# Optimization experiments

Hardware: AMD Instinct MI355X
Metric: run time of the kernel (lower is better)

Reference implementation:

```python
import jax, jax.numpy as jnp
import numpy as np

B, C, INTER, H, W = 4, 256, 128, 64, 64
EPS = 1e-5

def conv1x1(x, w, b):
    # x: [B,Cin,H,W], w: [Cout,Cin], b: [Cout]
    return jnp.einsum('bchw,oc->bohw', x, w) + b[None, :, None, None]

def setup_inputs() -> dict:
    key = jax.random.key(0)
    ks = jax.random.split(key, 12)
    sc_in = 1.0 / np.sqrt(C)
    sc_int = 1.0 / np.sqrt(INTER)
    return {
        'x': jax.random.normal(ks[0], (B, C, H, W), dtype=jnp.float32),
        'g_w': jax.random.normal(ks[1], (INTER, C), dtype=jnp.float32) * sc_in,
        'g_b': jax.random.normal(ks[2], (INTER,), dtype=jnp.float32) * 0.01,
        'theta_w': jax.random.normal(ks[3], (INTER, C), dtype=jnp.float32) * sc_in,
        'theta_b': jax.random.normal(ks[4], (INTER,), dtype=jnp.float32) * 0.01,
        'phi_w': jax.random.normal(ks[5], (INTER, C), dtype=jnp.float32) * sc_in,
        'phi_b': jax.random.normal(ks[6], (INTER,), dtype=jnp.float32) * 0.01,
        'w_w': jax.random.normal(ks[7], (C, INTER), dtype=jnp.float32) * sc_int,
        'w_b': jax.random.normal(ks[8], (C,), dtype=jnp.float32) * 0.01,
        'gamma': jax.random.normal(ks[9], (C,), dtype=jnp.float32) * 0.1 + 1.0,
        'beta': jax.random.normal(ks[10], (C,), dtype=jnp.float32) * 0.1,
    }

def reference(x, g_w, g_b, theta_w, theta_b, phi_w, phi_b, w_w, w_b, gamma, beta):
    b, c, h, w = x.shape
    n = h * w
    g_x = conv1x1(x, g_w, g_b).reshape(b, INTER, n).transpose(0, 2, 1)      # [b,n,d]
    theta_x = conv1x1(x, theta_w, theta_b).reshape(b, INTER, n).transpose(0, 2, 1)  # [b,n,d]
    phi_x = conv1x1(x, phi_w, phi_b).reshape(b, INTER, n)                   # [b,d,n]
    f = jnp.einsum('bnd,bdm->bnm', theta_x, phi_x)                          # [b,n,n]
    f_div_c = jax.nn.softmax(f, axis=-1)
    y = jnp.einsum('bnm,bmd->bnd', f_div_c, g_x)                            # [b,n,d]
    y = y.transpose(0, 2, 1).reshape(b, INTER, h, w)                        # [b,d,h,w]
    w_y = conv1x1(y, w_w, w_b)                                              # [b,c,h,w]
    # BatchNorm2d (training mode: batch statistics, biased variance)
    mean = jnp.mean(w_y, axis=(0, 2, 3), keepdims=True)
    var = jnp.var(w_y, axis=(0, 2, 3), keepdims=True)
    bn = (w_y - mean) * jax.lax.rsqrt(var + EPS)
    bn = bn * gamma[None, :, None, None] + beta[None, :, None, None]
    return bn + x
```

## Files before the change

kernel.cpp:

```cpp
#include <hip/hip_runtime.h>

#define B_ 4
#define C_ 256
#define D_ 128
#define N_ 4096
#define BN_ 16384

typedef unsigned short u16t;
typedef _Float16 f16t;
typedef f16t f16x8 __attribute__((ext_vector_type(8)));
typedef f16t f16x4 __attribute__((ext_vector_type(4)));
typedef float f32x4 __attribute__((ext_vector_type(4)));

static __device__ __forceinline__ u16t f2h(float f) {
  f16t h = (f16t)f; u16t u; __builtin_memcpy(&u, &h, 2); return u;
}
static __device__ __forceinline__ float h2f(u16t u) {
  f16t h; __builtin_memcpy(&h, &u, 2); return (float)h;
}

static __device__ __forceinline__ void gld_lds16(const u16t* g, u16t* l) {
  __builtin_amdgcn_global_load_lds(
      (const __attribute__((address_space(1))) void*)g,
      (__attribute__((address_space(3))) void*)l, 16, 0, 0);
}

__global__ __launch_bounds__(256) void transpose_prep(
    const float* __restrict__ x, u16t* __restrict__ xT,
    const float* __restrict__ th_w, const float* __restrict__ ph_w,
    const float* __restrict__ th_b, const float* __restrict__ ph_b,
    const float* __restrict__ g_w, const float* __restrict__ w_w,
    u16t* __restrict__ Wc, u16t* __restrict__ gwc, u16t* __restrict__ wwc,
    float* __restrict__ bc) {
  __shared__ u16t t[32][33];
  const int b = blockIdx.z, c0 = blockIdx.y * 32, n0 = blockIdx.x * 32;
  const int tid = threadIdx.x;
  {
    const int cl = tid >> 3, n4 = (tid & 7) * 4;
    const float4 v = *(const float4*)(x + ((size_t)b * C_ + c0 + cl) * N_ + n0 + n4);
    t[n4 + 0][cl] = f2h(v.x);
    t[n4 + 1][cl] = f2h(v.y);
    t[n4 + 2][cl] = f2h(v.z);
    t[n4 + 3][cl] = f2h(v.w);
  }
  __syncthreads();
  {
    const int nl = tid >> 3, c4 = (tid & 7) * 4;
    unsigned int lo = (unsigned int)t[nl][c4 + 0] | ((unsigned int)t[nl][c4 + 1] << 16);
    unsigned int hi = (unsigned int)t[nl][c4 + 2] | ((unsigned int)t[nl][c4 + 3] << 16);
    uint2 o; o.x = lo; o.y = hi;
    *(uint2*)(xT + ((size_t)b * N_ + n0 + nl) * C_ + c0 + c4) = o;
  }
  if (blockIdx.y == 0 && blockIdx.z == 0) {
    for (int idx = blockIdx.x * 256 + tid; idx < 131328; idx += 32768) {
      if (idx < 65536) {
        const int j = idx >> 8, c = idx & 255;
        const float v = (j < 128) ? th_w[j * 256 + c] : ph_w[(j - 128) * 256 + c];
        Wc[idx] = f2h(v);
      } else if (idx < 98304) {
        const int i = idx - 65536;
        gwc[i] = f2h(g_w[i]);
      } else if (idx < 131072) {
        const int i = idx - 98304;
        wwc[i] = f2h(w_w[i]);
      } else {
        const int j = idx - 131072;
        bc[j] = (j < 128) ? th_b[j] : ph_b[j - 128];
      }
    }
  }
}

__global__ __launch_bounds__(256)
void gemm_qkv(const u16t* __restrict__ xT, const u16t* __restrict__ Wc,
              const u16t* __restrict__ gwc, const float* __restrict__ bc,
              const float* __restrict__ g_b, u16t* __restrict__ QKo,
              u16t* __restrict__ Vo) {
  __shared__ __attribute__((aligned(16))) u16t lA[128 * 40];
  __shared__ __attribute__((aligned(16))) u16t lB[128 * 40];
  const int z = blockIdx.z, bx = blockIdx.x;
  const u16t* xTb = xT + (size_t)z * N_ * C_;
  const u16t* A; const u16t* B; u16t* Cb; int ldc, m0, j0, colb;
  const float* bias;
  if (bx < 64) {
    A = xTb; B = Wc; Cb = QKo + (size_t)z * N_ * 256; ldc = 256;
    m0 = (bx >> 1) * 128; j0 = (bx & 1) * 128; bias = bc; colb = 1;
  } else {
    A = gwc; B = xTb; Cb = Vo + (size_t)z * D_ * N_; ldc = N_;
    m0 = 0; j0 = (bx - 64) * 128; bias = g_b; colb = 0;
  }
  const int tid = threadIdx.x, lane = tid & 63, wave = tid >> 6;
  const int quad = lane >> 4, l16 = lane & 15;
  const int wm = wave & 1, wj = wave >> 1;

  const f32x4 zero = {0.f, 0.f, 0.f, 0.f};
  f32x4 acc[4][4];
#pragma unroll
  for (int mi = 0; mi < 4; ++mi)
#pragma unroll
    for (int ji = 0; ji < 4; ++ji) acc[mi][ji] = zero;

  for (int k0 = 0; k0 < 256; k0 += 32) {
#pragma unroll
    for (int rr = 0; rr < 2; ++rr) {
      const int idx = rr * 256 + tid;
      const int row = idx >> 2, sg = idx & 3;
      *(uint4*)&lA[row * 40 + sg * 8] = *(const uint4*)(A + (size_t)(m0 + row) * 256 + k0 + sg * 8);
      *(uint4*)&lB[row * 40 + sg * 8] = *(const uint4*)(B + (size_t)(j0 + row) * 256 + k0 + sg * 8);
    }
    __syncthreads();
    f16x8 af[4], bfr[4];
#pragma unroll
    for (int i = 0; i < 4; ++i)
      af[i] = *(const f16x8*)&lA[(wm * 64 + i * 16 + l16) * 40 + quad * 8];
#pragma unroll
    for (int i = 0; i < 4; ++i)
      bfr[i] = *(const f16x8*)&lB[(wj * 64 + i * 16 + l16) * 40 + quad * 8];
#pragma unroll
    for (int mi = 0; mi < 4; ++mi)
#pragma unroll
      for (int ji = 0; ji < 4; ++ji)
        acc[mi][ji] = __builtin_amdgcn_mfma_f32_16x16x32_f16(af[mi], bfr[ji], acc[mi][ji], 0, 0, 0);
    __syncthreads();
  }

  float cb[4];
  if (colb) {
#pragma unroll
    for (int ji = 0; ji < 4; ++ji) cb[ji] = bias[j0 + wj * 64 + ji * 16 + l16];
  }
#pragma unroll
  for (int mi = 0; mi < 4; ++mi) {
#pragma unroll
    for (int r = 0; r < 4; ++r) {
      const int row = m0 + wm * 64 + mi * 16 + quad * 4 + r;
      const float rb = colb ? 0.f : bias[row];
#pragma unroll
      for (int ji = 0; ji < 4; ++ji) {
        const int col = j0 + wj * 64 + ji * 16 + l16;
        const float v = acc[mi][ji][r] + (colb ? cb[ji] : rb);
        Cb[(size_t)row * ldc + col] = f2h(v);
      }
    }
  }
}

__global__ __launch_bounds__(256, 2)
void attn(const u16t* __restrict__ QK, const u16t* __restrict__ V,
          u16t* __restrict__ On0, u16t* __restrict__ On1, float* __restrict__ ml) {
  const int b = blockIdx.y;
  const int split = blockIdx.z;
  const int n0 = blockIdx.x * 128;
  const int kv0 = split * (N_ / 4);
  const int tid = threadIdx.x, lane = tid & 63, wave = tid >> 6;
  const int quad = lane >> 4, l16 = lane & 15;
  const int x7 = l16 & 7;
  __shared__ __attribute__((aligned(16))) u16t Ks[2][64 * 128];
  __shared__ __attribute__((aligned(16))) u16t Vs[2][128 * 64];
  const u16t* QKb = QK + (size_t)b * N_ * 256;
  const u16t* Vb  = V  + (size_t)b * D_ * N_;

  const int krow_l = lane >> 4, kchunk_l = lane & 15;
  const int vrow_l = lane >> 3, vchunk_l = lane & 7;

  f16x8 qf[2][4];
#pragma unroll
  for (int qi = 0; qi < 2; ++qi) {
    const u16t* qrow = QKb + (size_t)(n0 + wave * 32 + qi * 16 + l16) * 256;
#pragma unroll
    for (int kc = 0; kc < 4; ++kc)
      qf[qi][kc] = *(const f16x8*)(qrow + kc * 32 + quad * 8);
  }

  const f32x4 zero = {0.f, 0.f, 0.f, 0.f};
  f32x4 o[2][8];
#pragma unroll
  for (int qi = 0; qi < 2; ++qi)
#pragma unroll
    for (int db = 0; db < 8; ++db) o[qi][db] = zero;
  float m[2] = {-1e30f, -1e30f}, l[2] = {0.f, 0.f};

#pragma unroll
  for (int i = 0; i < 4; ++i) {
    const int krow = (wave * 4 + i) * 4 + krow_l;
    const int kcl = kchunk_l ^ (krow & 7);
    gld_lds16(QKb + (size_t)(kv0 + krow) * 256 + 128 + kcl * 8,
              &Ks[0][(wave * 4 + i) * 512]);
  }
#pragma unroll
  for (int i = 0; i < 4; ++i) {
    const int vrow = (wave * 4 + i) * 8 + vrow_l;
    const int vcl = vchunk_l ^ (vrow & 7);
    gld_lds16(Vb + (size_t)vrow * N_ + kv0 + vcl * 8,
              &Vs[0][(wave * 4 + i) * 512]);
  }
  __syncthreads();

  int cur = 0;
  for (int it = 0; it < 16; ++it) {
    if (it < 15) {
      const int kvn = kv0 + (it + 1) * 64;
#pragma unroll
      for (int i = 0; i < 4; ++i) {
        const int krow = (wave * 4 + i) * 4 + krow_l;
        const int kcl = kchunk_l ^ (krow & 7);
        gld_lds16(QKb + (size_t)(kvn + krow) * 256 + 128 + kcl * 8,
                  &Ks[cur ^ 1][(wave * 4 + i) * 512]);
      }
#pragma unroll
      for (int i = 0; i < 4; ++i) {
        const int vrow = (wave * 4 + i) * 8 + vrow_l;
        const int vcl = vchunk_l ^ (vrow & 7);
        gld_lds16(Vb + (size_t)vrow * N_ + kvn + vcl * 8,
                  &Vs[cur ^ 1][(wave * 4 + i) * 512]);
      }
    }

    const u16t* KsC = &Ks[cur][0];
    const u16t* VsC = &Vs[cur][0];

    f32x4 s[2][4];
#pragma unroll
    for (int qi = 0; qi < 2; ++qi)
#pragma unroll
      for (int ci = 0; ci < 4; ++ci) s[qi][ci] = zero;
#pragma unroll
    for (int kc = 0; kc < 4; ++kc) {
#pragma unroll
      for (int ci = 0; ci < 4; ++ci) {
        f16x8 kf = *(const f16x8*)&KsC[(ci * 16 + l16) * 128 + (((kc * 4 + quad) ^ x7) << 3)];
        s[0][ci] = __builtin_amdgcn_mfma_f32_16x16x32_f16(kf, qf[0][kc], s[0][ci], 0, 0, 0);
        s[1][ci] = __builtin_amdgcn_mfma_f32_16x16x32_f16(kf, qf[1][kc], s[1][ci], 0, 0, 0);
      }
    }

    f16x4 pb[2][4];
#pragma unroll
    for (int qi = 0; qi < 2; ++qi) {
      float m0_ = fmaxf(fmaxf(s[qi][0][0], s[qi][0][1]), fmaxf(s[qi][0][2], s[qi][0][3]));
      float m1_ = fmaxf(fmaxf(s[qi][1][0], s[qi][1][1]), fmaxf(s[qi][1][2], s[qi][1][3]));
      float m2_ = fmaxf(fmaxf(s[qi][2][0], s[qi][2][1]), fmaxf(s[qi][2][2], s[qi][2][3]));
      float m3_ = fmaxf(fmaxf(s[qi][3][0], s[qi][3][1]), fmaxf(s[qi][3][2], s[qi][3][3]));
      float mx = fmaxf(fmaxf(m0_, m1_), fmaxf(m2_, m3_));
      mx = fmaxf(mx, __shfl_xor(mx, 16));
      mx = fmaxf(mx, __shfl_xor(mx, 32));
      const bool defer = __all(mx <= m[qi] + 8.f);
      float mnew = m[qi];
      if (!defer) {
        mnew = fmaxf(m[qi], mx);
        const float alq = __expf(m[qi] - mnew);
        l[qi] *= alq;
#pragma unroll
        for (int db = 0; db < 8; ++db) {
#pragma unroll
          for (int r = 0; r < 4; ++r) o[qi][db][r] *= alq;
        }
        m[qi] = mnew;
      }
      float psum = 0.f;
#pragma unroll
      for (int ci = 0; ci < 4; ++ci) {
#pragma unroll
        for (int r = 0; r < 4; ++r) {
          const float p = __expf(s[qi][ci][r] - mnew);
          psum += p;
          pb[qi][ci][r] = (f16t)p;
        }
      }
      psum += __shfl_xor(psum, 16);
      psum += __shfl_xor(psum, 32);
      l[qi] += psum;
    }

#pragma unroll
    for (int ci = 0; ci < 4; ++ci) {
#pragma unroll
      for (int db = 0; db < 8; ++db) {
        f16x4 av = *(const f16x4*)&VsC[(db * 16 + l16) * 64 +
                                       (((ci * 2 + (quad >> 1)) ^ x7) << 3) + (quad & 1) * 4];
        o[0][db] = __builtin_amdgcn_mfma_f32_16x16x16f16(av, pb[0][ci], o[0][db], 0, 0, 0);
        o[1][db] = __builtin_amdgcn_mfma_f32_16x16x16f16(av, pb[1][ci], o[1][db], 0, 0, 0);
      }
    }
    __syncthreads();
    cur ^= 1;
  }

  u16t* Onb = (split < 2) ? On0 : On1;
  const int sp = split & 1;
#pragma unroll
  for (int qi = 0; qi < 2; ++qi) {
    const int q = n0 + wave * 32 + qi * 16 + l16;
    const float inv = 1.0f / l[qi];
    u16t* yrow = Onb + (((size_t)sp * B_ + b) * N_ + q) * D_;
#pragma unroll
    for (int db = 0; db < 8; ++db) {
      f16x4 pk;
#pragma unroll
      for (int r = 0; r < 4; ++r) pk[r] = (f16t)(o[qi][db][r] * inv);
      *(f16x4*)(yrow + db * 16 + quad * 4) = pk;
    }
    if (quad == 0) {
      float* mlp = ml + ((size_t)split * BN_ + (size_t)b * N_ + q) * 2;
      mlp[0] = m[qi]; mlp[1] = l[qi];
    }
  }
}

__global__ __launch_bounds__(256)
void gemm_wy(const u16t* __restrict__ wwc, const u16t* __restrict__ O0,
             const u16t* __restrict__ O2, const float* __restrict__ ml,
             u16t* __restrict__ wy, const float* __restrict__ w_b) {
  __shared__ __attribute__((aligned(16))) u16t lA[4][128 * 40];
  __shared__ __attribute__((aligned(16))) u16t lB[4][64 * 40];
  __shared__ float wrow[64][4];
  const int z = blockIdx.z;
  const int m0 = blockIdx.y * 128, j0 = blockIdx.x * 64;
  const int tid = threadIdx.x, lane = tid & 63, wave = tid >> 6;
  const int quad = lane >> 4, l16 = lane & 15;
  const int wm = wave & 1, wj = wave >> 1;
  const size_t halfO = (size_t)BN_ * D_;

  uint4 b0[4], b1[4], b2[4], b3[4];
#pragma unroll
  for (int cs = 0; cs < 4; ++cs) {
    const int cid = cs * 256 + tid;
    const int row = cid >> 4, sg = cid & 15;
    const size_t base = ((size_t)z * N_ + j0 + row) * D_ + sg * 8;
    b0[cs] = *(const uint4*)(O0 + base);
    b1[cs] = *(const uint4*)(O0 + halfO + base);
    b2[cs] = *(const uint4*)(O2 + base);
    b3[cs] = *(const uint4*)(O2 + halfO + base);
  }
  uint4 aw[8];
#pragma unroll
  for (int as = 0; as < 8; ++as) {
    const int cid = as * 256 + tid;
    const int row = cid >> 4, sg = cid & 15;
    aw[as] = *(const uint4*)(wwc + (size_t)(m0 + row) * 128 + sg * 8);
  }
  float mlv[8];
  if (tid < 64) {
    const int q = j0 + tid;
#pragma unroll
    for (int s = 0; s < 4; ++s) {
      mlv[2 * s]     = ml[((size_t)s * BN_ + (size_t)z * N_ + q) * 2];
      mlv[2 * s + 1] = ml[((size_t)s * BN_ + (size_t)z * N_ + q) * 2 + 1];
    }
  }
  if (tid < 64) {
    float mstar = -1e30f;
#pragma unroll
    for (int s = 0; s < 4; ++s) mstar = fmaxf(mstar, mlv[2 * s]);
    float w[4], wsum = 0.f;
#pragma unroll
    for (int s = 0; s < 4; ++s) { w[s] = __expf(mlv[2 * s] - mstar) * mlv[2 * s + 1]; wsum += w[s]; }
    const float inv = 1.0f / wsum;
#pragma unroll
    for (int s = 0; s < 4; ++s) wrow[tid][s] = w[s] * inv;
  }
#pragma unroll
  for (int as = 0; as < 8; ++as) {
    const int cid = as * 256 + tid;
    const int row = cid >> 4, sg = cid & 15;
    *(uint4*)&lA[sg >> 2][row * 40 + (sg & 3) * 8] = aw[as];
  }
  __syncthreads();
#pragma unroll
  for (int cs = 0; cs < 4; ++cs) {
    const int cid = cs * 256 + tid;
    const int row = cid >> 4, sg = cid & 15;
    const float w0 = wrow[row][0], w1 = wrow[row][1];
    const float w2 = wrow[row][2], w3 = wrow[row][3];
    const unsigned* p0 = &b0[cs].x; const unsigned* p1 = &b1[cs].x;
    const unsigned* p2 = &b2[cs].x; const unsigned* p3 = &b3[cs].x;
    uint4 y; unsigned* py = &y.x;
#pragma unroll
    for (int i = 0; i < 4; ++i) {
      const float lo = w0 * h2f((u16t)(p0[i] & 0xffff)) + w1 * h2f((u16t)(p1[i] & 0xffff)) +
                       w2 * h2f((u16t)(p2[i] & 0xffff)) + w3 * h2f((u16t)(p3[i] & 0xffff));
      const float hi = w0 * h2f((u16t)(p0[i] >> 16)) + w1 * h2f((u16t)(p1[i] >> 16)) +
                       w2 * h2f((u16t)(p2[i] >> 16)) + w3 * h2f((u16t)(p3[i] >> 16));
      py[i] = (unsigned)f2h(lo) | ((unsigned)f2h(hi) << 16);
    }
    *(uint4*)&lB[sg >> 2][row * 40 + (sg & 3) * 8] = y;
  }
  __syncthreads();

  const f32x4 zero = {0.f, 0.f, 0.f, 0.f};
  f32x4 acc[4][2];
#pragma unroll
  for (int mi = 0; mi < 4; ++mi)
#pragma unroll
    for (int ji = 0; ji < 2; ++ji) acc[mi][ji] = zero;
#pragma unroll
  for (int kc = 0; kc < 4; ++kc) {
    f16x8 af[4], bfr[2];
#pragma unroll
    for (int i = 0; i < 4; ++i)
      af[i] = *(const f16x8*)&lA[kc][(wm * 64 + i * 16 + l16) * 40 + quad * 8];
#pragma unroll
    for (int i = 0; i < 2; ++i)
      bfr[i] = *(const f16x8*)&lB[kc][(wj * 32 + i * 16 + l16) * 40 + quad * 8];
#pragma unroll
    for (int mi = 0; mi < 4; ++mi)
#pragma unroll
      for (int ji = 0; ji < 2; ++ji)
        acc[mi][ji] = __builtin_amdgcn_mfma_f32_16x16x32_f16(af[mi], bfr[ji], acc[mi][ji], 0, 0, 0);
  }

#pragma unroll
  for (int mi = 0; mi < 4; ++mi) {
#pragma unroll
    for (int r = 0; r < 4; ++r) {
      const int row = m0 + wm * 64 + mi * 16 + quad * 4 + r;
      const float rb = w_b[row];
#pragma unroll
      for (int ji = 0; ji < 2; ++ji) {
        const int col = j0 + wj * 32 + ji * 16 + l16;
        const float v = acc[mi][ji][r] + rb;
        wy[(size_t)z * C_ * N_ + (size_t)row * N_ + col] = f2h(v);
      }
    }
  }
}

__global__ __launch_bounds__(256) void bn_stats_fin(const u16t* __restrict__ wy,
                                                    const float* __restrict__ x,
                                                    const float* __restrict__ gamma,
                                                    const float* __restrict__ beta,
                                                    float* __restrict__ out) {
  const int c = blockIdx.x;
  const int tid = threadIdx.x, lane = tid & 63, wave = tid >> 6;
  __shared__ float red[8];
  __shared__ float mv[2];
  float s1 = 0.f, s2 = 0.f;
#pragma unroll
  for (int it = 0; it < 8; ++it) {
    const int e = (it * 256 + tid) * 8;
    const int z = e >> 12, n = e & 4095;
    const uint4 v = *(const uint4*)(wy + (size_t)z * C_ * N_ + (size_t)c * N_ + n);
    const unsigned* p = &v.x;
#pragma unroll
    for (int i = 0; i < 4; ++i) {
      const float lo = h2f((u16t)(p[i] & 0xffff));
      const float hi = h2f((u16t)(p[i] >> 16));
      s1 += lo + hi;
      s2 += lo * lo + hi * hi;
    }
  }
  s1 += __shfl_xor(s1, 1);  s2 += __shfl_xor(s2, 1);
  s1 += __shfl_xor(s1, 2);  s2 += __shfl_xor(s2, 2);
  s1 += __shfl_xor(s1, 4);  s2 += __shfl_xor(s2, 4);
  s1 += __shfl_xor(s1, 8);  s2 += __shfl_xor(s2, 8);
  s1 += __shfl_xor(s1, 16); s2 += __shfl_xor(s2, 16);
  s1 += __shfl_xor(s1, 32); s2 += __shfl_xor(s2, 32);
  if (lane == 0) { red[wave] = s1; red[4 + wave] = s2; }
  __syncthreads();
  if (tid == 0) {
    const float inv_n = 1.0f / 16384.0f;
    const float tot1 = red[0] + red[1] + red[2] + red[3];
    const float tot2 = red[4] + red[5] + red[6] + red[7];
    const float mean = tot1 * inv_n;
    const float var = tot2 * inv_n - mean * mean;
    mv[0] = mean;
    mv[1] = rsqrtf(var + 1e-5f);
  }
  __syncthreads();
  const float mean = mv[0], rs = mv[1];
  const float g = gamma[c], bt = beta[c];
#pragma unroll
  for (int it = 0; it < 16; ++it) {
    const int e4 = it * 256 + tid;
    const int z = e4 >> 10, n4 = (e4 & 1023) * 4;
    const size_t off = ((size_t)z * C_ + c) * N_ + n4;
    const uint2 wv = *(const uint2*)(wy + off);
    const float4 xv = *(const float4*)(x + off);
    float4 ov;
    ov.x = (h2f((u16t)(wv.x & 0xffff)) - mean) * rs * g + bt + xv.x;
    ov.y = (h2f((u16t)(wv.x >> 16))    - mean) * rs * g + bt + xv.y;
    ov.z = (h2f((u16t)(wv.y & 0xffff)) - mean) * rs * g + bt + xv.z;
    ov.w = (h2f((u16t)(wv.y >> 16))    - mean) * rs * g + bt + xv.w;
    *(float4*)(out + off) = ov;
  }
}

extern "C" void kernel_launch(void* const* d_in, const int* in_sizes, int n_in,
                              void* d_out, int out_size, void* d_ws, size_t ws_size,
                              hipStream_t stream) {
  const float* x     = (const float*)d_in[0];
  const float* g_w   = (const float*)d_in[1];
  const float* g_b   = (const float*)d_in[2];
  const float* th_w  = (const float*)d_in[3];
  const float* th_b  = (const float*)d_in[4];
  const float* ph_w  = (const float*)d_in[5];
  const float* ph_b  = (const float*)d_in[6];
  const float* w_w   = (const float*)d_in[7];
  const float* w_b   = (const float*)d_in[8];
  const float* gamma = (const float*)d_in[9];
  const float* beta  = (const float*)d_in[10];
  float* out = (float*)d_out;
  char* ws = (char*)d_ws;

  u16t* O0  = (u16t*)(ws);
  u16t* QK  = (u16t*)(ws + 8388608);
  u16t* wy  = (u16t*)(ws + 8388608);
  u16t* V   = (u16t*)(ws + 16777216);
  u16t* Wc  = (u16t*)(ws + 20971520);
  u16t* gwc = (u16t*)(ws + 21102592);
  u16t* wwc = (u16t*)(ws + 21168128);
  float* bc = (float*)(ws + 21233664);
  float* ml = (float*)(ws + 21236736);
  u16t* O2 = (u16t*)d_out;

  transpose_prep<<<dim3(128, 8, B_), dim3(256), 0, stream>>>(
      x, (u16t*)ws, th_w, ph_w, th_b, ph_b, g_w, w_w, Wc, gwc, wwc, bc);

  gemm_qkv<<<dim3(96, 1, B_), dim3(256), 0, stream>>>(
      (u16t*)ws, Wc, gwc, bc, g_b, QK, V);

  attn<<<dim3(32, B_, 4), dim3(256), 0, stream>>>(QK, V, O0, O2, ml);

  gemm_wy<<<dim3(64, 2, B_), dim3(256), 0, stream>>>(wwc, O0, O2, ml, wy, w_b);

  bn_stats_fin<<<dim3(256), dim3(256), 0, stream>>>(wy, x, gamma, beta, out);
}
```

Baseline: 167.7 us.

## Fuse all five stages into one cooperative persistent kernel with grid syncs

Result: slower. 432.7 us (+158.0%).

```diff
diff --git a/kernel.cpp b/kernel.cpp
--- a/kernel.cpp
+++ b/kernel.cpp
@@ -1,4 +1,7 @@
 #include <hip/hip_runtime.h>
+#include <hip/hip_cooperative_groups.h>
+
+namespace cg = cooperative_groups;
 
 #define B_ 4
 #define C_ 256
@@ -23,6 +26,463 @@
   __builtin_amdgcn_global_load_lds(
       (const __attribute__((address_space(1))) void*)g,
       (__attribute__((address_space(3))) void*)l, 16, 0, 0);
+}
+
+__global__ __launch_bounds__(256, 2) void mega(
+    const float* __restrict__ x,
+    const float* __restrict__ th_w, const float* __restrict__ ph_w,
+    const float* __restrict__ th_b, const float* __restrict__ ph_b,
+    const float* __restrict__ g_w, const float* __restrict__ g_b,
+    const float* __restrict__ w_w, const float* __restrict__ w_b,
+    const float* __restrict__ gamma, const float* __restrict__ beta,
+    float* out,
+    u16t* xT,
+    u16t* QK,
+    u16t* __restrict__ V,
+    u16t* __restrict__ Wc, u16t* __restrict__ gwc, u16t* __restrict__ wwc,
+    float* __restrict__ bc, float* __restrict__ ml,
+    u16t* O2) {
+  __shared__ __attribute__((aligned(16))) char smem[65536];
+  cg::grid_group gg = cg::this_grid();
+  const int fblk = blockIdx.x;
+  const int tid = threadIdx.x, lane = tid & 63, wave = tid >> 6;
+  const int quad = lane >> 4, l16 = lane & 15;
+  const int wm = wave & 1, wj = wave >> 1;
+  const f32x4 zero = {0.f, 0.f, 0.f, 0.f};
+
+  if (fblk < 128) {
+    for (int idx = fblk * 256 + tid; idx < 131328; idx += 32768) {
+      if (idx < 65536) {
+        const int j = idx >> 8, c = idx & 255;
+        const float v = (j < 128) ? th_w[j * 256 + c] : ph_w[(j - 128) * 256 + c];
+        Wc[idx] = f2h(v);
+      } else if (idx < 98304) {
+        gwc[idx - 65536] = f2h(g_w[idx - 65536]);
+      } else if (idx < 131072) {
+        wwc[idx - 98304] = f2h(w_w[idx - 98304]);
+      } else {
+        const int j = idx - 131072;
+        bc[j] = (j < 128) ? th_b[j] : ph_b[j - 128];
+      }
+    }
+  }
+  {
+    u16t (*t)[33] = (u16t (*)[33])smem;
+    for (int i = 0; i < 8; ++i) {
+      const int tt = i * 512 + fblk;
+      const int bx = tt & 127, by = (tt >> 7) & 7, bz = tt >> 10;
+      const int c0 = by * 32, n0 = bx * 32;
+      {
+        const int cl = tid >> 3, n4 = (tid & 7) * 4;
+        const float4 v = *(const float4*)(x + ((size_t)bz * C_ + c0 + cl) * N_ + n0 + n4);
+        t[n4 + 0][cl] = f2h(v.x);
+        t[n4 + 1][cl] = f2h(v.y);
+        t[n4 + 2][cl] = f2h(v.z);
+        t[n4 + 3][cl] = f2h(v.w);
+      }
+      __syncthreads();
+      {
+        const int nl = tid >> 3, c4 = (tid & 7) * 4;
+        unsigned lo = (unsigned)t[nl][c4 + 0] | ((unsigned)t[nl][c4 + 1] << 16);
+        unsigned hi = (unsigned)t[nl][c4 + 2] | ((unsigned)t[nl][c4 + 3] << 16);
+        uint2 o; o.x = lo; o.y = hi;
+        *(uint2*)(xT + ((size_t)bz * N_ + n0 + nl) * C_ + c0 + c4) = o;
+      }
+      __syncthreads();
+    }
+  }
+  gg.sync();
+
+  if (fblk < 384) {
+    u16t* lA = (u16t*)smem;
+    u16t* lB = (u16t*)(smem + 10240);
+    const int z = fblk / 96, bx = fblk % 96;
+    const u16t* xTb = xT + (size_t)z * N_ * C_;
+    const u16t* A; const u16t* B; u16t* Cb; int ldc, m0, j0, colb;
+    const float* bias;
+    if (bx < 64) {
+      A = xTb; B = Wc; Cb = QK + (size_t)z * N_ * 256; ldc = 256;
+      m0 = (bx >> 1) * 128; j0 = (bx & 1) * 128; bias = bc; colb = 1;
+    } else {
+      A = gwc; B = xTb; Cb = V + (size_t)z * D_ * N_; ldc = N_;
+      m0 = 0; j0 = (bx - 64) * 128; bias = g_b; colb = 0;
+    }
+    f32x4 acc[4][4];
+#pragma unroll
+    for (int mi = 0; mi < 4; ++mi)
+#pragma unroll
+      for (int ji = 0; ji < 4; ++ji) acc[mi][ji] = zero;
+
+    for (int k0 = 0; k0 < 256; k0 += 32) {
+#pragma unroll
+      for (int rr = 0; rr < 2; ++rr) {
+        const int idx = rr * 256 + tid;
+        const int row = idx >> 2, sg = idx & 3;
+        *(uint4*)&lA[row * 40 + sg * 8] = *(const uint4*)(A + (size_t)(m0 + row) * 256 + k0 + sg * 8);
+        *(uint4*)&lB[row * 40 + sg * 8] = *(const uint4*)(B + (size_t)(j0 + row) * 256 + k0 + sg * 8);
+      }
+      __syncthreads();
+      f16x8 af[4], bfr[4];
+#pragma unroll
+      for (int i = 0; i < 4; ++i)
+        af[i] = *(const f16x8*)&lA[(wm * 64 + i * 16 + l16) * 40 + quad * 8];
+#pragma unroll
+      for (int i = 0; i < 4; ++i)
+        bfr[i] = *(const f16x8*)&lB[(wj * 64 + i * 16 + l16) * 40 + quad * 8];
+#pragma unroll
+      for (int mi = 0; mi < 4; ++mi)
+#pragma unroll
+        for (int ji = 0; ji < 4; ++ji)
+          acc[mi][ji] = __builtin_amdgcn_mfma_f32_16x16x32_f16(af[mi], bfr[ji], acc[mi][ji], 0, 0, 0);
+      __syncthreads();
+    }
+
+    float cb[4];
+    if (colb) {
+#pragma unroll
+      for (int ji = 0; ji < 4; ++ji) cb[ji] = bias[j0 + wj * 64 + ji * 16 + l16];
+    }
+#pragma unroll
+    for (int mi = 0; mi < 4; ++mi) {
+#pragma unroll
+      for (int r = 0; r < 4; ++r) {
+        const int row = m0 + wm * 64 + mi * 16 + quad * 4 + r;
+        const float rb = colb ? 0.f : bias[row];
+#pragma unroll
+        for (int ji = 0; ji < 4; ++ji) {
+          const int col = j0 + wj * 64 + ji * 16 + l16;
+          const float v = acc[mi][ji][r] + (colb ? cb[ji] : rb);
+          Cb[(size_t)row * ldc + col] = f2h(v);
+        }
+      }
+    }
+  }
+  gg.sync();
+
+  {
+    u16t* Ksm = (u16t*)smem;
+    u16t* Vsm = (u16t*)(smem + 32768);
+    const int n0 = (fblk & 31) * 128;
+    const int ab = (fblk >> 5) & 3;
+    const int split = fblk >> 7;
+    const int kv0 = split * (N_ / 4);
+    const int x7 = l16 & 7;
+    const u16t* QKb = QK + (size_t)ab * N_ * 256;
+    const u16t* Vb  = V  + (size_t)ab * D_ * N_;
+    const int krow_l = lane >> 4, kchunk_l = lane & 15;
+    const int vrow_l = lane >> 3, vchunk_l = lane & 7;
+
+    f16x8 qf[2][4];
+#pragma unroll
+    for (int qi = 0; qi < 2; ++qi) {
+      const u16t* qrow = QKb + (size_t)(n0 + wave * 32 + qi * 16 + l16) * 256;
+#pragma unroll
+      for (int kc = 0; kc < 4; ++kc)
+        qf[qi][kc] = *(const f16x8*)(qrow + kc * 32 + quad * 8);
+    }
+
+    f32x4 o[2][8];
+#pragma unroll
+    for (int qi = 0; qi < 2; ++qi)
+#pragma unroll
+      for (int db = 0; db < 8; ++db) o[qi][db] = zero;
+    float m[2] = {-1e30f, -1e30f}, l[2] = {0.f, 0.f};
+
+#pragma unroll
+    for (int i = 0; i < 4; ++i) {
+      const int krow = (wave * 4 + i) * 4 + krow_l;
+      const int kcl = kchunk_l ^ (krow & 7);
+      gld_lds16(QKb + (size_t)(kv0 + krow) * 256 + 128 + kcl * 8,
+                Ksm + (wave * 4 + i) * 512);
+    }
+#pragma unroll
+    for (int i = 0; i < 4; ++i) {
+      const int vrow = (wave * 4 + i) * 8 + vrow_l;
+      const int vcl = vchunk_l ^ (vrow & 7);
+      gld_lds16(Vb + (size_t)vrow * N_ + kv0 + vcl * 8,
+                Vsm + (wave * 4 + i) * 512);
+    }
+    __syncthreads();
+
+    int cur = 0;
+    for (int it = 0; it < 16; ++it) {
+      if (it < 15) {
+        const int kvn = kv0 + (it + 1) * 64;
+#pragma unroll
+        for (int i = 0; i < 4; ++i) {
+          const int krow = (wave * 4 + i) * 4 + krow_l;
+          const int kcl = kchunk_l ^ (krow & 7);
+          gld_lds16(QKb + (size_t)(kvn + krow) * 256 + 128 + kcl * 8,
+                    Ksm + (cur ^ 1) * 8192 + (wave * 4 + i) * 512);
+        }
+#pragma unroll
+        for (int i = 0; i < 4; ++i) {
+          const int vrow = (wave * 4 + i) * 8 + vrow_l;
+          const int vcl = vchunk_l ^ (vrow & 7);
+          gld_lds16(Vb + (size_t)vrow * N_ + kvn + vcl * 8,
+                    Vsm + (cur ^ 1) * 8192 + (wave * 4 + i) * 512);
+        }
+      }
+
+      const u16t* KsC = Ksm + cur * 8192;
+      const u16t* VsC = Vsm + cur * 8192;
+
+      f32x4 s[2][4];
+#pragma unroll
+      for (int qi = 0; qi < 2; ++qi)
+#pragma unroll
+        for (int ci = 0; ci < 4; ++ci) s[qi][ci] = zero;
+#pragma unroll
+      for (int kc = 0; kc < 4; ++kc) {
+#pragma unroll
+        for (int ci = 0; ci < 4; ++ci) {
+          f16x8 kf = *(const f16x8*)&KsC[(ci * 16 + l16) * 128 + (((kc * 4 + quad) ^ x7) << 3)];
+          s[0][ci] = __builtin_amdgcn_mfma_f32_16x16x32_f16(kf, qf[0][kc], s[0][ci], 0, 0, 0);
+          s[1][ci] = __builtin_amdgcn_mfma_f32_16x16x32_f16(kf, qf[1][kc], s[1][ci], 0, 0, 0);
+        }
+      }
+
+      f16x4 pb[2][4];
+#pragma unroll
+      for (int qi = 0; qi < 2; ++qi) {
+        float m0_ = fmaxf(fmaxf(s[qi][0][0], s[qi][0][1]), fmaxf(s[qi][0][2], s[qi][0][3]));
+        float m1_ = fmaxf(fmaxf(s[qi][1][0], s[qi][1][1]), fmaxf(s[qi][1][2], s[qi][1][3]));
+        float m2_ = fmaxf(fmaxf(s[qi][2][0], s[qi][2][1]), fmaxf(s[qi][2][2], s[qi][2][3]));
+        float m3_ = fmaxf(fmaxf(s[qi][3][0], s[qi][3][1]), fmaxf(s[qi][3][2], s[qi][3][3]));
+        float mx = fmaxf(fmaxf(m0_, m1_), fmaxf(m2_, m3_));
+        mx = fmaxf(mx, __shfl_xor(mx, 16));
+        mx = fmaxf(mx, __shfl_xor(mx, 32));
+        const bool defer = __all(mx <= m[qi] + 8.f);
+        float mnew = m[qi];
+        if (!defer) {
+          mnew = fmaxf(m[qi], mx);
+          const float alq = __expf(m[qi] - mnew);
+          l[qi] *= alq;
+#pragma unroll
+          for (int db = 0; db < 8; ++db) {
+#pragma unroll
+            for (int r = 0; r < 4; ++r) o[qi][db][r] *= alq;
+          }
+          m[qi] = mnew;
+        }
+        float psum = 0.f;
+#pragma unroll
+        for (int ci = 0; ci < 4; ++ci) {
+#pragma unroll
+          for (int r = 0; r < 4; ++r) {
+            const float p = __expf(s[qi][ci][r] - mnew);
+            psum += p;
+            pb[qi][ci][r] = (f16t)p;
+          }
+        }
+        psum += __shfl_xor(psum, 16);
+        psum += __shfl_xor(psum, 32);
+        l[qi] += psum;
+      }
+
+#pragma unroll
+      for (int ci = 0; ci < 4; ++ci) {
+#pragma unroll
+        for (int db = 0; db < 8; ++db) {
+          f16x4 av = *(const f16x4*)&VsC[(db * 16 + l16) * 64 +
+                                         (((ci * 2 + (quad >> 1)) ^ x7) << 3) + (quad & 1) * 4];
+          o[0][db] = __builtin_amdgcn_mfma_f32_16x16x16f16(av, pb[0][ci], o[0][db], 0, 0, 0);
+          o[1][db] = __builtin_amdgcn_mfma_f32_16x16x16f16(av, pb[1][ci], o[1][db], 0, 0, 0);
+        }
+      }
+      __syncthreads();
+      cur ^= 1;
+    }
+
+    u16t* Onb = (split < 2) ? xT : O2;
+    const int sp = split & 1;
+#pragma unroll
+    for (int qi = 0; qi < 2; ++qi) {
+      const int q = n0 + wave * 32 + qi * 16 + l16;
+      const float inv = 1.0f / l[qi];
+      u16t* yrow = Onb + (((size_t)sp * B_ + ab) * N_ + q) * D_;
+#pragma unroll
+      for (int db = 0; db < 8; ++db) {
+        f16x4 pk;
+#pragma unroll
+        for (int r = 0; r < 4; ++r) pk[r] = (f16t)(o[qi][db][r] * inv);
+        *(f16x4*)(yrow + db * 16 + quad * 4) = pk;
+      }
+      if (quad == 0) {
+        float* mlp = ml + ((size_t)split * BN_ + (size_t)ab * N_ + q) * 2;
+        mlp[0] = m[qi]; mlp[1] = l[qi];
+      }
+    }
+  }
+  gg.sync();
+
+  {
+    u16t* lA = (u16t*)smem;
+    u16t* lB = (u16t*)(smem + 40960);
+    float* wrow = (float*)(smem + 61440);
+    const u16t* O0 = xT;
+    u16t* wy = QK;
+    const int z = fblk >> 7;
+    const int m0 = ((fblk >> 6) & 1) * 128, j0 = (fblk & 63) * 64;
+    const size_t halfO = (size_t)BN_ * D_;
+
+    uint4 b0[4], b1[4], b2[4], b3[4];
+#pragma unroll
+    for (int cs = 0; cs < 4; ++cs) {
+      const int cid = cs * 256 + tid;
+      const int row = cid >> 4, sg = cid & 15;
+      const size_t base = ((size_t)z * N_ + j0 + row) * D_ + sg * 8;
+      b0[cs] = *(const uint4*)(O0 + base);
+      b1[cs] = *(const uint4*)(O0 + halfO + base);
+      b2[cs] = *(const uint4*)(O2 + base);
+      b3[cs] = *(const uint4*)(O2 + halfO + base);
+    }
+    uint4 aw[8];
+#pragma unroll
+    for (int as = 0; as < 8; ++as) {
+      const int cid = as * 256 + tid;
+      const int row = cid >> 4, sg = cid & 15;
+      aw[as] = *(const uint4*)(wwc + (size_t)(m0 + row) * 128 + sg * 8);
+    }
+    float mlv[8];
+    if (tid < 64) {
+      const int q = j0 + tid;
+#pragma unroll
+      for (int s = 0; s < 4; ++s) {
+        mlv[2 * s]     = ml[((size_t)s * BN_ + (size_t)z * N_ + q) * 2];
+        mlv[2 * s + 1] = ml[((size_t)s * BN_ + (size_t)z * N_ + q) * 2 + 1];
+      }
+      float mstar = -1e30f;
+#pragma unroll
+      for (int s = 0; s < 4; ++s) mstar = fmaxf(mstar, mlv[2 * s]);
+      float w[4], wsum = 0.f;
+#pragma unroll
+      for (int s = 0; s < 4; ++s) { w[s] = __expf(mlv[2 * s] - mstar) * mlv[2 * s + 1]; wsum += w[s]; }
+      const float inv = 1.0f / wsum;
+#pragma unroll
+      for (int s = 0; s < 4; ++s) wrow[tid * 4 + s] = w[s] * inv;
+    }
+#pragma unroll
+    for (int as = 0; as < 8; ++as) {
+      const int cid = as * 256 + tid;
+      const int row = cid >> 4, sg = cid & 15;
+      *(uint4*)&lA[(sg >> 2) * 5120 + row * 40 + (sg & 3) * 8] = aw[as];
+    }
+    __syncthreads();
+#pragma unroll
+    for (int cs = 0; cs < 4; ++cs) {
+      const int cid = cs * 256 + tid;
+      const int row = cid >> 4, sg = cid & 15;
+      const float w0 = wrow[row * 4 + 0], w1 = wrow[row * 4 + 1];
+      const float w2 = wrow[row * 4 + 2], w3 = wrow[row * 4 + 3];
+      const unsigned* p0 = &b0[cs].x; const unsigned* p1 = &b1[cs].x;
+      const unsigned* p2 = &b2[cs].x; const unsigned* p3 = &b3[cs].x;
+      uint4 y; unsigned* py = &y.x;
+#pragma unroll
+      for (int i = 0; i < 4; ++i) {
+        const float lo = w0 * h2f((u16t)(p0[i] & 0xffff)) + w1 * h2f((u16t)(p1[i] & 0xffff)) +
+                         w2 * h2f((u16t)(p2[i] & 0xffff)) + w3 * h2f((u16t)(p3[i] & 0xffff));
+        const float hi = w0 * h2f((u16t)(p0[i] >> 16)) + w1 * h2f((u16t)(p1[i] >> 16)) +
+                         w2 * h2f((u16t)(p2[i] >> 16)) + w3 * h2f((u16t)(p3[i] >> 16));
+        py[i] = (unsigned)f2h(lo) | ((unsigned)f2h(hi) << 16);
+      }
+      *(uint4*)&lB[(sg >> 2) * 2560 + row * 40 + (sg & 3) * 8] = y;
+    }
+    __syncthreads();
+
+    f32x4 acc[4][2];
+#pragma unroll
+    for (int mi = 0; mi < 4; ++mi)
+#pragma unroll
+      for (int ji = 0; ji < 2; ++ji) acc[mi][ji] = zero;
+#pragma unroll
+    for (int kc = 0; kc < 4; ++kc) {
+      f16x8 af[4], bfr[2];
+#pragma unroll
+      for (int i = 0; i < 4; ++i)
+        af[i] = *(const f16x8*)&lA[kc * 5120 + (wm * 64 + i * 16 + l16) * 40 + quad * 8];
+#pragma unroll
+      for (int i = 0; i < 2; ++i)
+        bfr[i] = *(const f16x8*)&lB[kc * 2560 + (wj * 32 + i * 16 + l16) * 40 + quad * 8];
+#pragma unroll
+      for (int mi = 0; mi < 4; ++mi)
+#pragma unroll
+        for (int ji = 0; ji < 2; ++ji)
+          acc[mi][ji] = __builtin_amdgcn_mfma_f32_16x16x32_f16(af[mi], bfr[ji], acc[mi][ji], 0, 0, 0);
+    }
+
+#pragma unroll
+    for (int mi = 0; mi < 4; ++mi) {
+#pragma unroll
+      for (int r = 0; r < 4; ++r) {
+        const int row = m0 + wm * 64 + mi * 16 + quad * 4 + r;
+        const float rb = w_b[row];
+#pragma unroll
+        for (int ji = 0; ji < 2; ++ji) {
+          const int col = j0 + wj * 32 + ji * 16 + l16;
+          const float v = acc[mi][ji][r] + rb;
+          wy[(size_t)z * C_ * N_ + (size_t)row * N_ + col] = f2h(v);
+        }
+      }
+    }
+  }
+  gg.sync();
+
+  if (fblk < 256) {
+    const u16t* wy = QK;
+    float* red = (float*)smem;
+    float* mvs = (float*)(smem + 32);
+    const int c = fblk;
+    float s1 = 0.f, s2 = 0.f;
+#pragma unroll
+    for (int it = 0; it < 8; ++it) {
+      const int e = (it * 256 + tid) * 8;
+      const int z = e >> 12, n = e & 4095;
+      const uint4 v = *(const uint4*)(wy + (size_t)z * C_ * N_ + (size_t)c * N_ + n);
+      const unsigned* p = &v.x;
+#pragma unroll
+      for (int i = 0; i < 4; ++i) {
+        const float lo = h2f((u16t)(p[i] & 0xffff));
+        const float hi = h2f((u16t)(p[i] >> 16));
+        s1 += lo + hi;
+        s2 += lo * lo + hi * hi;
+      }
+    }
+    s1 += __shfl_xor(s1, 1);  s2 += __shfl_xor(s2, 1);
+    s1 += __shfl_xor(s1, 2);  s2 += __shfl_xor(s2, 2);
+    s1 += __shfl_xor(s1, 4);  s2 += __shfl_xor(s2, 4);
+    s1 += __shfl_xor(s1, 8);  s2 += __shfl_xor(s2, 8);
+    s1 += __shfl_xor(s1, 16); s2 += __shfl_xor(s2, 16);
+    s1 += __shfl_xor(s1, 32); s2 += __shfl_xor(s2, 32);
+    if (lane == 0) { red[wave] = s1; red[4 + wave] = s2; }
+    __syncthreads();
+    if (tid == 0) {
+      const float inv_n = 1.0f / 16384.0f;
+      const float tot1 = red[0] + red[1] + red[2] + red[3];
+      const float tot2 = red[4] + red[5] + red[6] + red[7];
+      const float mean = tot1 * inv_n;
+      const float var = tot2 * inv_n - mean * mean;
+      mvs[0] = mean;
+      mvs[1] = rsqrtf(var + 1e-5f);
+    }
+    __syncthreads();
+    const float mean = mvs[0], rs = mvs[1];
+    const float g = gamma[c], bt = beta[c];
+#pragma unroll
+    for (int it = 0; it < 16; ++it) {
+      const int e4 = it * 256 + tid;
+      const int z = e4 >> 10, n4 = (e4 & 1023) * 4;
+      const size_t off = ((size_t)z * C_ + c) * N_ + n4;
+      const uint2 wv = *(const uint2*)(wy + off);
+      const float4 xv = *(const float4*)(x + off);
+      float4 ov;
+      ov.x = (h2f((u16t)(wv.x & 0xffff)) - mean) * rs * g + bt + xv.x;
+      ov.y = (h2f((u16t)(wv.x >> 16))    - mean) * rs * g + bt + xv.y;
+      ov.z = (h2f((u16t)(wv.y & 0xffff)) - mean) * rs * g + bt + xv.z;
+      ov.w = (h2f((u16t)(wv.y >> 16))    - mean) * rs * g + bt + xv.w;
+      *(float4*)(out + off) = ov;
+    }
+  }
 }
 
 __global__ __launch_bounds__(256) void transpose_prep(
@@ -58,11 +518,9 @@
         const float v = (j < 128) ? th_w[j * 256 + c] : ph_w[(j - 128) * 256 + c];
         Wc[idx] = f2h(v);
       } else if (idx < 98304) {
-        const int i = idx - 65536;
-        gwc[i] = f2h(g_w[i]);
+        gwc[idx - 65536] = f2h(g_w[idx - 65536]);
       } else if (idx < 131072) {
-        const int i = idx - 98304;
-        wwc[i] = f2h(w_w[i]);
+        wwc[idx - 98304] = f2h(w_w[idx - 98304]);
       } else {
         const int j = idx - 131072;
         bc[j] = (j < 128) ? th_b[j] : ph_b[j - 128];
@@ -347,8 +805,6 @@
       mlv[2 * s]     = ml[((size_t)s * BN_ + (size_t)z * N_ + q) * 2];
       mlv[2 * s + 1] = ml[((size_t)s * BN_ + (size_t)z * N_ + q) * 2 + 1];
     }
-  }
-  if (tid < 64) {
     float mstar = -1e30f;
 #pragma unroll
     for (int s = 0; s < 4; ++s) mstar = fmaxf(mstar, mlv[2 * s]);
@@ -502,26 +958,34 @@
   float* out = (float*)d_out;
   char* ws = (char*)d_ws;
 
-  u16t* O0  = (u16t*)(ws);
+  u16t* xT  = (u16t*)(ws);
   u16t* QK  = (u16t*)(ws + 8388608);
-  u16t* wy  = (u16t*)(ws + 8388608);
   u16t* V   = (u16t*)(ws + 16777216);
   u16t* Wc  = (u16t*)(ws + 20971520);
   u16t* gwc = (u16t*)(ws + 21102592);
   u16t* wwc = (u16t*)(ws + 21168128);
   float* bc = (float*)(ws + 21233664);
   float* ml = (float*)(ws + 21236736);
-  u16t* O2 = (u16t*)d_out;
-
-  transpose_prep<<<dim3(128, 8, B_), dim3(256), 0, stream>>>(
-      x, (u16t*)ws, th_w, ph_w, th_b, ph_b, g_w, w_w, Wc, gwc, wwc, bc);
-
-  gemm_qkv<<<dim3(96, 1, B_), dim3(256), 0, stream>>>(
-      (u16t*)ws, Wc, gwc, bc, g_b, QK, V);
-
-  attn<<<dim3(32, B_, 4), dim3(256), 0, stream>>>(QK, V, O0, O2, ml);
-
-  gemm_wy<<<dim3(64, 2, B_), dim3(256), 0, stream>>>(wwc, O0, O2, ml, wy, w_b);
-
-  bn_stats_fin<<<dim3(256), dim3(256), 0, stream>>>(wy, x, gamma, beta, out);
+  u16t* O2  = (u16t*)d_out;
+
+  void* args[] = {
+    (void*)&x,
+    (void*)&th_w, (void*)&ph_w, (void*)&th_b, (void*)&ph_b,
+    (void*)&g_w, (void*)&g_b, (void*)&w_w, (void*)&w_b,
+    (void*)&gamma, (void*)&beta,
+    (void*)&out,
+    (void*)&xT, (void*)&QK, (void*)&V,
+    (void*)&Wc, (void*)&gwc, (void*)&wwc,
+    (void*)&bc, (void*)&ml, (void*)&O2,
+  };
+  hipError_t rc = hipLaunchCooperativeKernel((const void*)mega, dim3(512), dim3(256),
+                                             args, 0, stream);
+  if (rc != hipSuccess) {
+    transpose_prep<<<dim3(128, 8, B_), dim3(256), 0, stream>>>(
+        x, xT, th_w, ph_w, th_b, ph_b, g_w, w_w, Wc, gwc, wwc, bc);
+    gemm_qkv<<<dim3(96, 1, B_), dim3(256), 0, stream>>>(xT, Wc, gwc, bc, g_b, QK, V);
+    attn<<<dim3(32, B_, 4), dim3(256), 0, stream>>>(QK, V, xT, O2, ml);
+    gemm_wy<<<dim3(64, 2, B_), dim3(256), 0, stream>>>(wwc, xT, O2, ml, QK, w_b);
+    bn_stats_fin<<<dim3(256), dim3(256), 0, stream>>>(QK, x, gamma, beta, out);
+  }
 }
```
